# Optimization experiments

Measured on AMD Instinct MI355X. Metric: run time of the kernel, lower is better.

Reference implementation:

```python
import jax, jax.numpy as jnp
import numpy as np

B, T, C, H = 4, 2048, 1024, 64


def setup_inputs() -> dict:
    key = jax.random.key(0)
    kx, kk, kq, kv = jax.random.split(key, 4)
    scale = 1.0 / np.sqrt(C)
    return {
        "x": jax.random.normal(kx, (B, T, C), dtype=jnp.float32),
        "Wk": jax.random.normal(kk, (C, H), dtype=jnp.float32) * scale,
        "Wq": jax.random.normal(kq, (C, H), dtype=jnp.float32) * scale,
        "Wv": jax.random.normal(kv, (C, H), dtype=jnp.float32) * scale,
    }


def reference(x, Wk, Wq, Wv):
    # projections: [B, T, H]
    k = jnp.einsum("btc,ch->bth", x, Wk)
    q = jnp.einsum("btc,ch->bth", x, Wq)
    v = jnp.einsum("btc,ch->bth", x, Wv)
    # attention scores [B, T, T], scaled by sqrt(head_size)
    scores = jnp.einsum("bqh,bkh->bqk", q, k) / jnp.sqrt(jnp.asarray(H, x.dtype))
    # causal mask (decoder)
    causal = jnp.tril(jnp.ones((T, T), dtype=bool))
    scores = jnp.where(causal, scores, -jnp.inf)
    attn = jax.nn.softmax(scores, axis=-1)
    # dropout p=0.0 (eval) -> identity
    return jnp.einsum("bqk,bkh->bqh", attn, v)
```

## Files before the change

kernel.cpp:

```cpp
#include <hip/hip_runtime.h>
#include <hip/hip_bf16.h>

#define BB 4
#define TT 2048
#define CC 1024
#define HH 64
#define LOG2E 1.4426950408889634f
#define QSCALE (0.125f * LOG2E)

typedef __attribute__((ext_vector_type(8))) unsigned short ushort8;
typedef __attribute__((ext_vector_type(4))) unsigned short ushort4v;
typedef __attribute__((ext_vector_type(8))) __bf16 bf16x8;
typedef __attribute__((ext_vector_type(4))) float float4v;

static __device__ __forceinline__ unsigned short f2bf(float f) {
    return __builtin_bit_cast(unsigned short, (__bf16)f);
}

static __device__ __forceinline__ float4v mfma16(ushort8 a, ushort8 b, float4v c) {
    return __builtin_amdgcn_mfma_f32_16x16x32_bf16(
        __builtin_bit_cast(bf16x8, a), __builtin_bit_cast(bf16x8, b), c, 0, 0, 0);
}

static __device__ __forceinline__ ushort8 cvt8(float4v a, float4v b) {
    ushort8 r;
#pragma unroll
    for (int i = 0; i < 4; ++i) { r[i] = f2bf(a[i]); r[4 + i] = f2bf(b[i]); }
    return r;
}

#define BARRIER()                                            \
    do {                                                     \
        asm volatile("s_waitcnt lgkmcnt(0)" ::: "memory");   \
        __builtin_amdgcn_s_barrier();                        \
        asm volatile("" ::: "memory");                       \
    } while (0)

__global__ __launch_bounds__(256) void wconv_kernel(
    const float* __restrict__ Wq, const float* __restrict__ Wk,
    const float* __restrict__ Wv, unsigned short* __restrict__ wf)
{
    __shared__ __align__(16) float wsT[3][64][68];
    const int kc = blockIdx.x / 6, part = blockIdx.x % 6;
    const int t = threadIdx.x;
    const int r = t >> 2, c0 = (t & 3) << 4;
    const float* Ws[3] = {Wq, Wk, Wv};
#pragma unroll
    for (int y = 0; y < 3; ++y) {
        const float* src = Ws[y] + (size_t)(kc * 64 + r) * HH + c0;
        const float sc = (y == 0) ? QSCALE : 1.0f;
#pragma unroll
        for (int i = 0; i < 16; ++i) wsT[y][c0 + i][r] = src[i] * sc;
    }
    __syncthreads();
    const int U = part * 256 + t;
    const int lane = U & 63, qq = U >> 6;
    const int nt = qq % 12, ks = qq / 12;
    const int y = nt >> 2;
    const int col = 16 * (nt & 3) + (lane & 15);
    const int kl = ks * 32 + 8 * (lane >> 4);
    float4v v0 = *(const float4v*)&wsT[y][col][kl];
    float4v v1 = *(const float4v*)&wsT[y][col][kl + 4];
    *(ushort8*)&wf[((size_t)kc * 1536 + U) * 8] = cvt8(v0, v1);
}

__global__ __launch_bounds__(768) void proj_kernel(
    const float* __restrict__ x, const unsigned short* __restrict__ wf,
    unsigned short* __restrict__ qo, unsigned short* __restrict__ ko,
    unsigned short* __restrict__ vo)
{
    __shared__ __align__(16) unsigned short xa[2][2048];

    const int t0 = blockIdx.x << 5;
    const int tid = threadIdx.x;
    const int w = tid >> 6;
    const int lane = tid & 63;
    const int l15 = lane & 15, g = lane >> 4;

    const bool stg = tid < 256;
    const int sr = tid >> 3, su = tid & 7;
    const int soff = (sr * 8 + (su ^ (sr & 7))) * 8;
    const float* xp = x + (size_t)(t0 + sr) * CC + su * 8;

    float4v xr[4][2];
    if (stg) {
#pragma unroll
        for (int p = 0; p < 4; ++p) {
            xr[p][0] = *(const float4v*)(xp + p * 64);
            xr[p][1] = *(const float4v*)(xp + p * 64 + 4);
        }
    }

    const unsigned short* wfp = wf + ((size_t)w * 64 + lane) * 8;
    ushort8 bc0 = *(const ushort8*)(wfp);
    ushort8 bc1 = *(const ushort8*)(wfp + 6144);
    ushort8 bn0 = *(const ushort8*)(wfp + 2 * 6144);
    ushort8 bn1 = *(const ushort8*)(wfp + 3 * 6144);

    if (stg) *(ushort8*)&xa[0][soff] = cvt8(xr[0][0], xr[0][1]);
    BARRIER();

    const int sw = l15 & 7;
    const int r00 = (l15 * 8 + (g ^ sw)) * 8;
    const int r01 = (l15 * 8 + ((4 + g) ^ sw)) * 8;
    const int r10 = ((16 + l15) * 8 + (g ^ sw)) * 8;
    const int r11 = ((16 + l15) * 8 + ((4 + g) ^ sw)) * 8;

    float4v ac0 = (float4v)0.0f, ac1 = (float4v)0.0f;

#pragma unroll
    for (int kc = 0; kc < 16; ++kc) {
        const int cur = kc & 1;
        if (stg && kc + 4 < 16) {
            xr[kc & 3][0] = *(const float4v*)(xp + (kc + 4) * 64);
            xr[kc & 3][1] = *(const float4v*)(xp + (kc + 4) * 64 + 4);
        }
        ushort8 nw0, nw1;
        if (kc + 2 < 16) {
            nw0 = *(const ushort8*)(wfp + (size_t)(2 * kc + 4) * 6144);
            nw1 = *(const ushort8*)(wfp + (size_t)(2 * kc + 5) * 6144);
        }
        const unsigned short* xb = xa[cur];
        ushort8 a00 = *(const ushort8*)&xb[r00];
        ushort8 a01 = *(const ushort8*)&xb[r01];
        ushort8 a10 = *(const ushort8*)&xb[r10];
        ushort8 a11 = *(const ushort8*)&xb[r11];
        if (w < 8) {
            ac0 = mfma16(a00, bc0, ac0);
            ac0 = mfma16(a01, bc1, ac0);
            ac1 = mfma16(a10, bc0, ac1);
            ac1 = mfma16(a11, bc1, ac1);
        } else {
            ac0 = mfma16(bc0, a00, ac0);
            ac0 = mfma16(bc1, a01, ac0);
            ac1 = mfma16(bc0, a10, ac1);
            ac1 = mfma16(bc1, a11, ac1);
        }
        if (stg && kc + 1 < 16)
            *(ushort8*)&xa[cur ^ 1][soff] =
                cvt8(xr[(kc + 1) & 3][0], xr[(kc + 1) & 3][1]);
        BARRIER();
        bc0 = bn0; bc1 = bn1;
        if (kc + 2 < 16) { bn0 = nw0; bn1 = nw1; }
    }

    if (w < 8) {
        unsigned short* dst = (w < 4) ? qo : ko;
        const int nf = w & 3;
#pragma unroll
        for (int mt = 0; mt < 2; ++mt) {
            float4v a = mt ? ac1 : ac0;
#pragma unroll
            for (int r = 0; r < 4; ++r)
                dst[(size_t)(t0 + 16 * mt + 4 * g + r) * HH + 16 * nf + l15] =
                    f2bf(a[r]);
        }
    } else {
        const int nf = w - 8;
        const int b = t0 >> 11, tl = t0 & (TT - 1);
#pragma unroll
        for (int mt = 0; mt < 2; ++mt) {
            float4v a = mt ? ac1 : ac0;
#pragma unroll
            for (int r = 0; r < 4; ++r)
                vo[((size_t)b * HH + 16 * nf + 4 * g + r) * TT + tl + 16 * mt + l15] =
                    f2bf(a[r]);
        }
    }
}

__global__ __launch_bounds__(512, 2) void attn_kernel(
    const unsigned short* __restrict__ qw,
    const unsigned short* __restrict__ kw,
    const unsigned short* __restrict__ vw,
    float* __restrict__ out)
{
    __shared__ float om[8][16];
    __shared__ float olg[8][4][16];
    __shared__ __align__(16) float oo[8][16][64];

    const int idx = blockIdx.x;
    const int b = idx & (BB - 1);
    const int qt = (TT / 16 - 1) - (idx >> 2);
    const int q0 = qt << 4;
    const int tid = threadIdx.x;
    const int w = tid >> 6;
    const int lane = tid & 63;
    const int l15 = lane & 15;
    const int g = lane >> 4;
    const int q = q0 + l15;

    const unsigned short* qrow = qw + (size_t)(b * TT + q) * HH + 8 * g;
    ushort8 qf0 = *(const ushort8*)qrow;
    ushort8 qf1 = *(const ushort8*)(qrow + 32);

    const unsigned short* kb = kw + (size_t)b * TT * HH;
    const unsigned short* vb = vw + (size_t)b * HH * TT;

    float m_run = -3.0e38f, l_run = 0.0f;
    float4v o[4];
#pragma unroll
    for (int i = 0; i < 4; ++i) o[i] = (float4v)0.0f;

    for (int kv0 = 64 * w; kv0 < q0 + 16; kv0 += 512) {
        const unsigned short* kr = kb + (size_t)(kv0 + l15) * HH + 8 * g;
        ushort8 akl[4], akh[4];
#pragma unroll
        for (int f = 0; f < 4; ++f) {
            akl[f] = *(const ushort8*)(kr + f * 16 * HH);
            akh[f] = *(const ushort8*)(kr + f * 16 * HH + 32);
        }
        ushort8 av[4][2];
#pragma unroll
        for (int ht = 0; ht < 4; ++ht) {
            const unsigned short* vp = vb + (size_t)(16 * ht + l15) * TT + kv0 + 4 * g;
#pragma unroll
            for (int g2 = 0; g2 < 2; ++g2) {
                ushort4v v0 = *(const ushort4v*)(vp + 32 * g2);
                ushort4v v1 = *(const ushort4v*)(vp + 32 * g2 + 16);
#pragma unroll
                for (int r = 0; r < 4; ++r) {
                    av[ht][g2][r] = v0[r];
                    av[ht][g2][4 + r] = v1[r];
                }
            }
        }

        float4v s[4];
#pragma unroll
        for (int f = 0; f < 4; ++f) {
            s[f] = mfma16(akl[f], qf0, (float4v)0.0f);
            s[f] = mfma16(akh[f], qf1, s[f]);
        }

        if (kv0 + 63 > q0) {
#pragma unroll
            for (int f = 0; f < 4; ++f)
#pragma unroll
                for (int r = 0; r < 4; ++r)
                    if (kv0 + 16 * f + 4 * g + r > q) s[f][r] = -1e30f;
        }

        float mt = s[0][0];
#pragma unroll
        for (int f = 0; f < 4; ++f)
#pragma unroll
            for (int r = 0; r < 4; ++r) mt = fmaxf(mt, s[f][r]);
        mt = fmaxf(mt, __shfl_xor(mt, 16, 64));
        mt = fmaxf(mt, __shfl_xor(mt, 32, 64));

        const float m_new = fmaxf(m_run, mt);
        const float scale = exp2f(m_run - m_new);
        float sum = 0.0f;
#pragma unroll
        for (int f = 0; f < 4; ++f)
#pragma unroll
            for (int r = 0; r < 4; ++r) {
                s[f][r] = exp2f(s[f][r] - m_new);
                sum += s[f][r];
            }
        l_run = l_run * scale + sum;
        m_run = m_new;
#pragma unroll
        for (int i = 0; i < 4; ++i) o[i] *= scale;

        ushort8 bp[2];
#pragma unroll
        for (int r = 0; r < 4; ++r) {
            bp[0][r] = f2bf(s[0][r]); bp[0][4 + r] = f2bf(s[1][r]);
            bp[1][r] = f2bf(s[2][r]); bp[1][4 + r] = f2bf(s[3][r]);
        }
#pragma unroll
        for (int ht = 0; ht < 4; ++ht) {
            o[ht] = mfma16(av[ht][0], bp[0], o[ht]);
            o[ht] = mfma16(av[ht][1], bp[1], o[ht]);
        }
    }

    if (lane < 16) om[w][lane] = m_run;
    olg[w][g][l15] = l_run;
#pragma unroll
    for (int ht = 0; ht < 4; ++ht)
        *(float4v*)&oo[w][l15][16 * ht + 4 * g] = o[ht];
    __syncthreads();

#pragma unroll 2
    for (int e = tid; e < 16 * HH; e += 512) {
        const int qq = e >> 6, h = e & 63;
        float mstar = om[0][qq];
#pragma unroll
        for (int w2 = 1; w2 < 8; ++w2) mstar = fmaxf(mstar, om[w2][qq]);
        float lsum = 0.0f, osum = 0.0f;
#pragma unroll
        for (int w2 = 0; w2 < 8; ++w2) {
            const float al = exp2f(om[w2][qq] - mstar);
            const float lw = olg[w2][0][qq] + olg[w2][1][qq] +
                             olg[w2][2][qq] + olg[w2][3][qq];
            lsum += al * lw;
            osum += al * oo[w2][qq][h];
        }
        out[((size_t)b * TT + q0 + qq) * HH + h] = osum / lsum;
    }
}

extern "C" void kernel_launch(void* const* d_in, const int* in_sizes, int n_in,
                              void* d_out, int out_size, void* d_ws, size_t ws_size,
                              hipStream_t stream) {
    const float* x  = (const float*)d_in[0];
    const float* Wk = (const float*)d_in[1];
    const float* Wq = (const float*)d_in[2];
    const float* Wv = (const float*)d_in[3];

    unsigned short* q_ws  = (unsigned short*)d_ws;
    unsigned short* k_ws  = q_ws + (size_t)BB * TT * HH;
    unsigned short* vt_ws = k_ws + (size_t)BB * TT * HH;
    unsigned short* wf_ws = vt_ws + (size_t)BB * TT * HH;

    wconv_kernel<<<96, 256, 0, stream>>>(Wq, Wk, Wv, wf_ws);
    proj_kernel<<<BB * TT / 32, 768, 0, stream>>>(x, wf_ws, q_ws, k_ws, vt_ws);
    attn_kernel<<<BB * TT / 16, 512, 0, stream>>>(q_ws, k_ws, vt_ws, (float*)d_out);
}
```

Baseline: 55.13 us.

## Pair causal query tiles per attention block and shrink projection tiles

The attention kernel now handles two query tiles per block, a long one from the end and a short one from the start, so every block gets about the same causal work and the grid is halved. The projection kernel switches to 16-row tiles with 384 threads, and each wave computes two output column tiles instead of two row tiles. This doubles the projection grid and reuses each loaded x fragment across two weight tiles. The cost is an extra barrier per phase in attention and serial work inside each attention block.

```diff
diff --git a/kernel.cpp b/kernel.cpp
--- a/kernel.cpp
+++ b/kernel.cpp
@@ -64,20 +64,21 @@
     *(ushort8*)&wf[((size_t)kc * 1536 + U) * 8] = cvt8(v0, v1);
 }
 
-__global__ __launch_bounds__(768) void proj_kernel(
+__global__ __launch_bounds__(384) void proj_kernel(
     const float* __restrict__ x, const unsigned short* __restrict__ wf,
     unsigned short* __restrict__ qo, unsigned short* __restrict__ ko,
     unsigned short* __restrict__ vo)
 {
-    __shared__ __align__(16) unsigned short xa[2][2048];
-
-    const int t0 = blockIdx.x << 5;
+    __shared__ __align__(16) unsigned short xa[2][1024];
+
+    const int t0 = blockIdx.x << 4;
     const int tid = threadIdx.x;
     const int w = tid >> 6;
     const int lane = tid & 63;
     const int l15 = lane & 15, g = lane >> 4;
-
-    const bool stg = tid < 256;
+    const int nt0 = 2 * w;
+
+    const bool stg = tid < 128;
     const int sr = tid >> 3, su = tid & 7;
     const int soff = (sr * 8 + (su ^ (sr & 7))) * 8;
     const float* xp = x + (size_t)(t0 + sr) * CC + su * 8;
@@ -91,11 +92,15 @@
         }
     }
 
-    const unsigned short* wfp = wf + ((size_t)w * 64 + lane) * 8;
-    ushort8 bc0 = *(const ushort8*)(wfp);
-    ushort8 bc1 = *(const ushort8*)(wfp + 6144);
-    ushort8 bn0 = *(const ushort8*)(wfp + 2 * 6144);
-    ushort8 bn1 = *(const ushort8*)(wfp + 3 * 6144);
+    const unsigned short* wp = wf + ((size_t)nt0 * 64 + lane) * 8;
+    ushort8 bc[2][2], bn[2][2];
+#pragma unroll
+    for (int ks = 0; ks < 2; ++ks)
+#pragma unroll
+        for (int j = 0; j < 2; ++j) {
+            bc[j][ks] = *(const ushort8*)(wp + (size_t)ks * 6144 + j * 512);
+            bn[j][ks] = *(const ushort8*)(wp + (size_t)(2 + ks) * 6144 + j * 512);
+        }
 
     if (stg) *(ushort8*)&xa[0][soff] = cvt8(xr[0][0], xr[0][1]);
     BARRIER();
@@ -103,10 +108,9 @@
     const int sw = l15 & 7;
     const int r00 = (l15 * 8 + (g ^ sw)) * 8;
     const int r01 = (l15 * 8 + ((4 + g) ^ sw)) * 8;
-    const int r10 = ((16 + l15) * 8 + (g ^ sw)) * 8;
-    const int r11 = ((16 + l15) * 8 + ((4 + g) ^ sw)) * 8;
-
-    float4v ac0 = (float4v)0.0f, ac1 = (float4v)0.0f;
+
+    float4v acc[2];
+    acc[0] = (float4v)0.0f; acc[1] = (float4v)0.0f;
 
 #pragma unroll
     for (int kc = 0; kc < 16; ++kc) {
@@ -115,56 +119,62 @@
             xr[kc & 3][0] = *(const float4v*)(xp + (kc + 4) * 64);
             xr[kc & 3][1] = *(const float4v*)(xp + (kc + 4) * 64 + 4);
         }
-        ushort8 nw0, nw1;
+        ushort8 nw[2][2];
         if (kc + 2 < 16) {
-            nw0 = *(const ushort8*)(wfp + (size_t)(2 * kc + 4) * 6144);
-            nw1 = *(const ushort8*)(wfp + (size_t)(2 * kc + 5) * 6144);
-        }
-        const unsigned short* xb = xa[cur];
-        ushort8 a00 = *(const ushort8*)&xb[r00];
-        ushort8 a01 = *(const ushort8*)&xb[r01];
-        ushort8 a10 = *(const ushort8*)&xb[r10];
-        ushort8 a11 = *(const ushort8*)&xb[r11];
-        if (w < 8) {
-            ac0 = mfma16(a00, bc0, ac0);
-            ac0 = mfma16(a01, bc1, ac0);
-            ac1 = mfma16(a10, bc0, ac1);
-            ac1 = mfma16(a11, bc1, ac1);
+#pragma unroll
+            for (int ks = 0; ks < 2; ++ks)
+#pragma unroll
+                for (int j = 0; j < 2; ++j)
+                    nw[j][ks] = *(const ushort8*)
+                        (wp + (size_t)(2 * kc + 4 + ks) * 6144 + j * 512);
+        }
+        ushort8 a0 = *(const ushort8*)&xa[cur][r00];
+        ushort8 a1 = *(const ushort8*)&xa[cur][r01];
+        if (w < 4) {
+#pragma unroll
+            for (int j = 0; j < 2; ++j) {
+                acc[j] = mfma16(a0, bc[j][0], acc[j]);
+                acc[j] = mfma16(a1, bc[j][1], acc[j]);
+            }
         } else {
-            ac0 = mfma16(bc0, a00, ac0);
-            ac0 = mfma16(bc1, a01, ac0);
-            ac1 = mfma16(bc0, a10, ac1);
-            ac1 = mfma16(bc1, a11, ac1);
+#pragma unroll
+            for (int j = 0; j < 2; ++j) {
+                acc[j] = mfma16(bc[j][0], a0, acc[j]);
+                acc[j] = mfma16(bc[j][1], a1, acc[j]);
+            }
         }
         if (stg && kc + 1 < 16)
             *(ushort8*)&xa[cur ^ 1][soff] =
                 cvt8(xr[(kc + 1) & 3][0], xr[(kc + 1) & 3][1]);
         BARRIER();
-        bc0 = bn0; bc1 = bn1;
-        if (kc + 2 < 16) { bn0 = nw0; bn1 = nw1; }
-    }
-
-    if (w < 8) {
-        unsigned short* dst = (w < 4) ? qo : ko;
-        const int nf = w & 3;
-#pragma unroll
-        for (int mt = 0; mt < 2; ++mt) {
-            float4v a = mt ? ac1 : ac0;
+#pragma unroll
+        for (int ks = 0; ks < 2; ++ks)
+#pragma unroll
+            for (int j = 0; j < 2; ++j) {
+                bc[j][ks] = bn[j][ks];
+                if (kc + 2 < 16) bn[j][ks] = nw[j][ks];
+            }
+    }
+
+    if (w < 4) {
+        unsigned short* dst = (w < 2) ? qo : ko;
+#pragma unroll
+        for (int j = 0; j < 2; ++j) {
+            const int nf = (nt0 + j) & 3;
 #pragma unroll
             for (int r = 0; r < 4; ++r)
-                dst[(size_t)(t0 + 16 * mt + 4 * g + r) * HH + 16 * nf + l15] =
-                    f2bf(a[r]);
+                dst[(size_t)(t0 + 4 * g + r) * HH + 16 * nf + l15] =
+                    f2bf(acc[j][r]);
         }
     } else {
-        const int nf = w - 8;
         const int b = t0 >> 11, tl = t0 & (TT - 1);
 #pragma unroll
-        for (int mt = 0; mt < 2; ++mt) {
-            float4v a = mt ? ac1 : ac0;
+        for (int j = 0; j < 2; ++j) {
+            const int nf = nt0 + j - 8;
 #pragma unroll
             for (int r = 0; r < 4; ++r)
-                vo[((size_t)b * HH + 16 * nf + 4 * g + r) * TT + tl + 16 * mt + l15] =
-                    f2bf(a[r]);
+                vo[((size_t)b * HH + 16 * nf + 4 * g + r) * TT + tl + l15] =
+                    f2bf(acc[j][r]);
         }
     }
 }
@@ -181,125 +191,131 @@
 
     const int idx = blockIdx.x;
     const int b = idx & (BB - 1);
-    const int qt = (TT / 16 - 1) - (idx >> 2);
-    const int q0 = qt << 4;
+    const int j = idx >> 2;
     const int tid = threadIdx.x;
     const int w = tid >> 6;
     const int lane = tid & 63;
     const int l15 = lane & 15;
     const int g = lane >> 4;
-    const int q = q0 + l15;
-
-    const unsigned short* qrow = qw + (size_t)(b * TT + q) * HH + 8 * g;
-    ushort8 qf0 = *(const ushort8*)qrow;
-    ushort8 qf1 = *(const ushort8*)(qrow + 32);
 
     const unsigned short* kb = kw + (size_t)b * TT * HH;
     const unsigned short* vb = vw + (size_t)b * HH * TT;
 
-    float m_run = -3.0e38f, l_run = 0.0f;
-    float4v o[4];
-#pragma unroll
-    for (int i = 0; i < 4; ++i) o[i] = (float4v)0.0f;
-
-    for (int kv0 = 64 * w; kv0 < q0 + 16; kv0 += 512) {
-        const unsigned short* kr = kb + (size_t)(kv0 + l15) * HH + 8 * g;
-        ushort8 akl[4], akh[4];
-#pragma unroll
-        for (int f = 0; f < 4; ++f) {
-            akl[f] = *(const ushort8*)(kr + f * 16 * HH);
-            akh[f] = *(const ushort8*)(kr + f * 16 * HH + 32);
-        }
-        ushort8 av[4][2];
-#pragma unroll
-        for (int ht = 0; ht < 4; ++ht) {
-            const unsigned short* vp = vb + (size_t)(16 * ht + l15) * TT + kv0 + 4 * g;
-#pragma unroll
-            for (int g2 = 0; g2 < 2; ++g2) {
-                ushort4v v0 = *(const ushort4v*)(vp + 32 * g2);
-                ushort4v v1 = *(const ushort4v*)(vp + 32 * g2 + 16);
+    for (int ph = 0; ph < 2; ++ph) {
+        const int qt = ph ? j : (TT / 16 - 1) - j;
+        const int q0 = qt << 4;
+        const int q = q0 + l15;
+
+        const unsigned short* qrow = qw + (size_t)(b * TT + q) * HH + 8 * g;
+        ushort8 qf0 = *(const ushort8*)qrow;
+        ushort8 qf1 = *(const ushort8*)(qrow + 32);
+
+        float m_run = -3.0e38f, l_run = 0.0f;
+        float4v o[4];
+#pragma unroll
+        for (int i = 0; i < 4; ++i) o[i] = (float4v)0.0f;
+
+        for (int kv0 = 64 * w; kv0 < q0 + 16; kv0 += 512) {
+            const unsigned short* kr = kb + (size_t)(kv0 + l15) * HH + 8 * g;
+            ushort8 akl[4], akh[4];
+#pragma unroll
+            for (int f = 0; f < 4; ++f) {
+                akl[f] = *(const ushort8*)(kr + f * 16 * HH);
+                akh[f] = *(const ushort8*)(kr + f * 16 * HH + 32);
+            }
+            ushort8 av[4][2];
+#pragma unroll
+            for (int ht = 0; ht < 4; ++ht) {
+                const unsigned short* vp =
+                    vb + (size_t)(16 * ht + l15) * TT + kv0 + 4 * g;
+#pragma unroll
+                for (int g2 = 0; g2 < 2; ++g2) {
+                    ushort4v v0 = *(const ushort4v*)(vp + 32 * g2);
+                    ushort4v v1 = *(const ushort4v*)(vp + 32 * g2 + 16);
+#pragma unroll
+                    for (int r = 0; r < 4; ++r) {
+                        av[ht][g2][r] = v0[r];
+                        av[ht][g2][4 + r] = v1[r];
+                    }
+                }
+            }
+
+            float4v s[4];
+#pragma unroll
+            for (int f = 0; f < 4; ++f) {
+                s[f] = mfma16(akl[f], qf0, (float4v)0.0f);
+                s[f] = mfma16(akh[f], qf1, s[f]);
+            }
+
+            if (kv0 + 63 > q0) {
+#pragma unroll
+                for (int f = 0; f < 4; ++f)
+#pragma unroll
+                    for (int r = 0; r < 4; ++r)
+                        if (kv0 + 16 * f + 4 * g + r > q) s[f][r] = -1e30f;
+            }
+
+            float mt = s[0][0];
+#pragma unroll
+            for (int f = 0; f < 4; ++f)
+#pragma unroll
+                for (int r = 0; r < 4; ++r) mt = fmaxf(mt, s[f][r]);
+            mt = fmaxf(mt, __shfl_xor(mt, 16, 64));
+            mt = fmaxf(mt, __shfl_xor(mt, 32, 64));
+
+            const float m_new = fmaxf(m_run, mt);
+            const float scale = exp2f(m_run - m_new);
+            float sum = 0.0f;
+#pragma unroll
+            for (int f = 0; f < 4; ++f)
 #pragma unroll
                 for (int r = 0; r < 4; ++r) {
-                    av[ht][g2][r] = v0[r];
-                    av[ht][g2][4 + r] = v1[r];
+                    s[f][r] = exp2f(s[f][r] - m_new);
+                    sum += s[f][r];
                 }
-            }
-        }
-
-        float4v s[4];
-#pragma unroll
-        for (int f = 0; f < 4; ++f) {
-            s[f] = mfma16(akl[f], qf0, (float4v)0.0f);
-            s[f] = mfma16(akh[f], qf1, s[f]);
-        }
-
-        if (kv0 + 63 > q0) {
-#pragma unroll
-            for (int f = 0; f < 4; ++f)
-#pragma unroll
-                for (int r = 0; r < 4; ++r)
-                    if (kv0 + 16 * f + 4 * g + r > q) s[f][r] = -1e30f;
-        }
-
-        float mt = s[0][0];
-#pragma unroll
-        for (int f = 0; f < 4; ++f)
-#pragma unroll
-            for (int r = 0; r < 4; ++r) mt = fmaxf(mt, s[f][r]);
-        mt = fmaxf(mt, __shfl_xor(mt, 16, 64));
-        mt = fmaxf(mt, __shfl_xor(mt, 32, 64));
-
-        const float m_new = fmaxf(m_run, mt);
-        const float scale = exp2f(m_run - m_new);
-        float sum = 0.0f;
-#pragma unroll
-        for (int f = 0; f < 4; ++f)
+            l_run = l_run * scale + sum;
+            m_run = m_new;
+#pragma unroll
+            for (int i = 0; i < 4; ++i) o[i] *= scale;
+
+            ushort8 bp[2];
 #pragma unroll
             for (int r = 0; r < 4; ++r) {
-                s[f][r] = exp2f(s[f][r] - m_new);
-                sum += s[f][r];
-            }
-        l_run = l_run * scale + sum;
-        m_run = m_new;
-#pragma unroll
-        for (int i = 0; i < 4; ++i) o[i] *= scale;
-
-        ushort8 bp[2];
-#pragma unroll
-        for (int r = 0; r < 4; ++r) {
-            bp[0][r] = f2bf(s[0][r]); bp[0][4 + r] = f2bf(s[1][r]);
-            bp[1][r] = f2bf(s[2][r]); bp[1][4 + r] = f2bf(s[3][r]);
-        }
-#pragma unroll
-        for (int ht = 0; ht < 4; ++ht) {
-            o[ht] = mfma16(av[ht][0], bp[0], o[ht]);
-            o[ht] = mfma16(av[ht][1], bp[1], o[ht]);
-        }
-    }
-
-    if (lane < 16) om[w][lane] = m_run;
-    olg[w][g][l15] = l_run;
-#pragma unroll
-    for (int ht = 0; ht < 4; ++ht)
-        *(float4v*)&oo[w][l15][16 * ht + 4 * g] = o[ht];
-    __syncthreads();
+                bp[0][r] = f2bf(s[0][r]); bp[0][4 + r] = f2bf(s[1][r]);
+                bp[1][r] = f2bf(s[2][r]); bp[1][4 + r] = f2bf(s[3][r]);
+            }
+#pragma unroll
+            for (int ht = 0; ht < 4; ++ht) {
+                o[ht] = mfma16(av[ht][0], bp[0], o[ht]);
+                o[ht] = mfma16(av[ht][1], bp[1], o[ht]);
+            }
+        }
+
+        if (lane < 16) om[w][lane] = m_run;
+        olg[w][g][l15] = l_run;
+#pragma unroll
+        for (int ht = 0; ht < 4; ++ht)
+            *(float4v*)&oo[w][l15][16 * ht + 4 * g] = o[ht];
+        __syncthreads();
 
 #pragma unroll 2
-    for (int e = tid; e < 16 * HH; e += 512) {
-        const int qq = e >> 6, h = e & 63;
-        float mstar = om[0][qq];
-#pragma unroll
-        for (int w2 = 1; w2 < 8; ++w2) mstar = fmaxf(mstar, om[w2][qq]);
-        float lsum = 0.0f, osum = 0.0f;
-#pragma unroll
-        for (int w2 = 0; w2 < 8; ++w2) {
-            const float al = exp2f(om[w2][qq] - mstar);
-            const float lw = olg[w2][0][qq] + olg[w2][1][qq] +
-                             olg[w2][2][qq] + olg[w2][3][qq];
-            lsum += al * lw;
-            osum += al * oo[w2][qq][h];
-        }
-        out[((size_t)b * TT + q0 + qq) * HH + h] = osum / lsum;
+        for (int e = tid; e < 16 * HH; e += 512) {
+            const int qq = e >> 6, h = e & 63;
+            float mstar = om[0][qq];
+#pragma unroll
+            for (int w2 = 1; w2 < 8; ++w2) mstar = fmaxf(mstar, om[w2][qq]);
+            float lsum = 0.0f, osum = 0.0f;
+#pragma unroll
+            for (int w2 = 0; w2 < 8; ++w2) {
+                const float al = exp2f(om[w2][qq] - mstar);
+                const float lw = olg[w2][0][qq] + olg[w2][1][qq] +
+                                 olg[w2][2][qq] + olg[w2][3][qq];
+                lsum += al * lw;
+                osum += al * oo[w2][qq][h];
+            }
+            out[((size_t)b * TT + q0 + qq) * HH + h] = osum / lsum;
+        }
+        __syncthreads();
     }
 }
 
@@ -317,6 +333,6 @@
     unsigned short* wf_ws = vt_ws + (size_t)BB * TT * HH;
 
     wconv_kernel<<<96, 256, 0, stream>>>(Wq, Wk, Wv, wf_ws);
-    proj_kernel<<<BB * TT / 32, 768, 0, stream>>>(x, wf_ws, q_ws, k_ws, vt_ws);
-    attn_kernel<<<BB * TT / 16, 512, 0, stream>>>(q_ws, k_ws, vt_ws, (float*)d_out);
-}
+    proj_kernel<<<BB * TT / 16, 384, 0, stream>>>(x, wf_ws, q_ws, k_ws, vt_ws);
+    attn_kernel<<<BB * TT / 32, 512, 0, stream>>>(q_ws, k_ws, vt_ws, (float*)d_out);
+}
```

After: 50.33 us. 8.7% less time.
